# Performance work log

Measured on AMD Instinct MI355X. Metric: run time of the kernel, lower is better.

## Reference

```python
import jax, jax.numpy as jnp
import numpy as np

GAMMA = 0.99


def setup_inputs() -> dict:
    key = jax.random.key(0)
    ks = jax.random.split(key, 6)
    T, D, H = 65536, 1024, 1024
    s1 = 1.0 / np.sqrt(D)
    s2 = 1.0 / np.sqrt(H)
    return {
        "rewards": jax.random.normal(ks[0], (T,), jnp.float32),
        "obs": jax.random.normal(ks[1], (T, D), jnp.float32),
        "W1": jax.random.normal(ks[2], (D, H), jnp.float32) * s1,
        "b1": jnp.zeros((H,), jnp.float32),
        "W2": jax.random.normal(ks[3], (H, H), jnp.float32) * s2,
        "b2": jnp.zeros((H,), jnp.float32),
        "W3": jax.random.normal(ks[4], (H, 1), jnp.float32) * s2,
        "b3": jnp.zeros((1,), jnp.float32),
    }


def _discounted_returns(rewards):
    # G[i] = r[i] + gamma * G[i+1], computed as a reverse scan
    def step(g, r):
        g = r + GAMMA * g
        return g, g
    _, G = jax.lax.scan(step, jnp.zeros((), rewards.dtype), rewards, reverse=True)
    return G


def reference(rewards, obs, W1, b1, W2, b2, W3, b3):
    G = _discounted_returns(rewards)              # [T]
    h = jax.nn.relu(obs @ W1 + b1)                # [T, H]
    h = jax.nn.relu(h @ W2 + b2)                  # [T, H]
    V = (h @ W3 + b3).reshape(-1)                 # [T]
    return G - V
```

## Files before the change

### kernel.cpp

```cpp
#include <hip/hip_runtime.h>

typedef __bf16 bf16x8 __attribute__((ext_vector_type(8)));
typedef __bf16 bf16x4 __attribute__((ext_vector_type(4)));
typedef float  f32x4  __attribute__((ext_vector_type(4)));

#define GAMMA 0.99f

__device__ __forceinline__ void gload_lds16(const void* g, void* l) {
  __builtin_amdgcn_global_load_lds(
      (const __attribute__((address_space(1))) void*)g,
      (__attribute__((address_space(3))) void*)l, 16, 0, 0);
}

#define VMCNT0() asm volatile("s_waitcnt vmcnt(0)" ::: "memory")
#define BAR() __builtin_amdgcn_s_barrier()
#define MFMA(d, a, b) d = __builtin_amdgcn_mfma_f32_16x16x32_bf16(a, b, d, 0, 0, 0)

__global__ __launch_bounds__(1024) void mega_prep(
    const float* __restrict__ rw, float* __restrict__ G,
    const float* __restrict__ obs, __bf16* __restrict__ obsb,
    const float* __restrict__ W1, const float* __restrict__ W2,
    __bf16* __restrict__ BT1, __bf16* __restrict__ BT2, int nObs) {
  __shared__ float smem[4224];
  const int blk = blockIdx.x;
  const int t = threadIdx.x;
  if (blk == 0) {
    float* sv = smem;
    const float4* rp = (const float4*)(rw + t * 64);
    float4 lv[16];
#pragma unroll
    for (int i = 0; i < 16; ++i) lv[i] = rp[i];
    float loc[64];
#pragma unroll
    for (int i = 0; i < 16; ++i) {
      loc[4 * i + 0] = lv[i].x; loc[4 * i + 1] = lv[i].y;
      loc[4 * i + 2] = lv[i].z; loc[4 * i + 3] = lv[i].w;
    }
    float g = 0.f;
#pragma unroll
    for (int j = 63; j >= 0; --j) { g = loc[j] + GAMMA * g; loc[j] = g; }
    sv[t] = g;
    float W = GAMMA;
#pragma unroll
    for (int i = 0; i < 6; ++i) W *= W;
    float v = g;
    for (int s = 1; s < 1024; s <<= 1) {
      __syncthreads();
      float o = (t + s < 1024) ? sv[t + s] : 0.f;
      __syncthreads();
      v += W * o;
      sv[t] = v;
      W *= W;
    }
    __syncthreads();
    const float nxt = (t < 1023) ? sv[t + 1] : 0.f;
    float pw = GAMMA;
#pragma unroll
    for (int j = 63; j >= 0; --j) {
      G[t * 64 + j] = loc[j] + pw * nxt;
      pw *= GAMMA;
    }
  } else if (blk <= nObs) {
    const size_t base = (size_t)(blk - 1) * 32768 + (size_t)t * 8;
#pragma unroll
    for (int it = 0; it < 4; ++it) {
      const size_t e = base + (size_t)it * 8192;
      float4 u0 = *(const float4*)(obs + e);
      float4 u1 = *(const float4*)(obs + e + 4);
      bf16x8 o = {(__bf16)u0.x, (__bf16)u0.y, (__bf16)u0.z, (__bf16)u0.w,
                  (__bf16)u1.x, (__bf16)u1.y, (__bf16)u1.z, (__bf16)u1.w};
      *(bf16x8*)(obsb + e) = o;
    }
  } else {
    const int sub = t >> 8, tt = t & 255;
    const int wi = (blk - nObs - 1) * 4 + sub;
    const float* W = (wi >= 1024) ? W2 : W1;
    __bf16* O = (wi >= 1024) ? BT2 : BT1;
    const int tile = wi & 1023;
    const int ti = tile >> 5, tj = tile & 31;
    float* s = smem + sub * 1056;
    const int rr = tt >> 3, c4 = (tt & 7) * 4;
    float4 v = *(const float4*)(W + (size_t)(ti * 32 + rr) * 1024 + tj * 32 + c4);
    s[rr * 33 + c4 + 0] = v.x; s[rr * 33 + c4 + 1] = v.y;
    s[rr * 33 + c4 + 2] = v.z; s[rr * 33 + c4 + 3] = v.w;
    __syncthreads();
    bf16x4 o = {(__bf16)s[(c4 + 0) * 33 + rr], (__bf16)s[(c4 + 1) * 33 + rr],
                (__bf16)s[(c4 + 2) * 33 + rr], (__bf16)s[(c4 + 3) * 33 + rr]};
    *(bf16x4*)(O + (size_t)(tj * 32 + rr) * 1024 + ti * 32 + c4) = o;
  }
}

#define GEMM_KLOOP(APTR, BPTR)                                                 \
  extern __shared__ char lds[];                                                \
  const int t = threadIdx.x, lane = t & 63, w = t >> 6;                        \
  const int wsr = w >> 2, wsc = w & 3, g = lane >> 4, l15 = lane & 15;         \
  const int bid = blockIdx.x;                                                  \
  const int mb = (bid & 7) * 32 + ((bid >> 3) >> 2);                           \
  const int nb = (bid >> 3) & 3;                                               \
  const size_t stg_off =                                                       \
      (size_t)(t >> 2) * 2048 + (size_t)(((t & 3) ^ ((t >> 3) & 3)) * 16);     \
  const char* Ag = (const char*)(APTR) + (size_t)mb * 524288 + stg_off;        \
  const char* Bg = (const char*)(BPTR) + (size_t)nb * 524288 + stg_off;        \
  const int csw = (g ^ ((l15 >> 1) & 3)) << 4;                                 \
  const int arb = (wsr * 64 + l15) * 64 + csw;                                 \
  const int brb = (wsc * 32 + l15) * 64 + csw + 16384;                         \
  f32x4 acc[2][4][2][2];                                                       \
  const f32x4 zero = {0.f, 0.f, 0.f, 0.f};                                     \
  _Pragma("unroll") for (int a_ = 0; a_ < 2; ++a_)                             \
  _Pragma("unroll") for (int b_ = 0; b_ < 4; ++b_)                             \
  _Pragma("unroll") for (int c_ = 0; c_ < 2; ++c_)                             \
  _Pragma("unroll") for (int d_ = 0; d_ < 2; ++d_)                             \
    acc[a_][b_][c_][d_] = zero;                                                \
  auto STA = [&](int buf, int kt) {                                            \
    const char* s = Ag + kt * 64;                                              \
    char* d = lds + buf * 32768 + t * 16;                                      \
    gload_lds16(s, d);                                                         \
    gload_lds16(s + 262144, d + 8192);                                         \
  };                                                                           \
  auto STB = [&](int buf, int kt) {                                            \
    const char* s = Bg + kt * 64;                                              \
    char* d = lds + buf * 32768 + 16384 + t * 16;                              \
    gload_lds16(s, d);                                                         \
    gload_lds16(s + 262144, d + 8192);                                         \
  };                                                                           \
  STA(0, 0);                                                                   \
  STB(0, 0);                                                                   \
  VMCNT0();                                                                    \
  BAR();                                                                       \
  int cur = 0;                                                                 \
  for (int kt = 0; kt < 32; ++kt) {                                            \
    const int nx = cur ^ 1;                                                    \
    const char* ab = lds + cur * 32768;                                        \
    if (kt < 31) STA(nx, kt + 1);                                              \
    bf16x8 bfr[2][2];                                                          \
    _Pragma("unroll") for (int nh = 0; nh < 2; ++nh)                           \
    _Pragma("unroll") for (int j = 0; j < 2; ++j)                              \
      bfr[nh][j] = *(const bf16x8*)(ab + brb + (nh * 128 + j * 16) * 64);      \
    if (kt < 31) STB(nx, kt + 1);                                              \
    bf16x8 afr[4];                                                             \
    _Pragma("unroll") for (int i = 0; i < 4; ++i)                              \
      afr[i] = *(const bf16x8*)(ab + arb + (i * 16) * 64);                     \
    __builtin_amdgcn_s_setprio(1);                                             \
    _Pragma("unroll") for (int i = 0; i < 4; ++i)                              \
    _Pragma("unroll") for (int nh = 0; nh < 2; ++nh)                           \
    _Pragma("unroll") for (int j = 0; j < 2; ++j)                              \
      MFMA(acc[0][i][nh][j], bfr[nh][j], afr[i]);                              \
    __builtin_amdgcn_s_setprio(0);                                             \
    _Pragma("unroll") for (int i = 0; i < 4; ++i)                              \
      afr[i] = *(const bf16x8*)(ab + arb + ((128 + i * 16) * 64));             \
    __builtin_amdgcn_s_setprio(1);                                             \
    _Pragma("unroll") for (int i = 0; i < 4; ++i)                              \
    _Pragma("unroll") for (int nh = 0; nh < 2; ++nh)                           \
    _Pragma("unroll") for (int j = 0; j < 2; ++j)                              \
      MFMA(acc[1][i][nh][j], bfr[nh][j], afr[i]);                              \
    __builtin_amdgcn_s_setprio(0);                                             \
    if (kt < 31) VMCNT0();                                                     \
    BAR();                                                                     \
    cur = nx;                                                                  \
  }

__global__ __launch_bounds__(512, 2) void gemm1(
    const __bf16* __restrict__ obsb, const __bf16* __restrict__ BT1,
    const float* __restrict__ b1, __bf16* __restrict__ h1) {
  GEMM_KLOOP(obsb, BT1)
  f32x4 b1q[2][2];
#pragma unroll
  for (int nh = 0; nh < 2; ++nh)
#pragma unroll
    for (int j = 0; j < 2; ++j)
      b1q[nh][j] =
          *(const f32x4*)(b1 + nb * 256 + nh * 128 + wsc * 32 + j * 16 + g * 4);
#pragma unroll
  for (int mh = 0; mh < 2; ++mh)
#pragma unroll
    for (int i = 0; i < 4; ++i) {
      const size_t mrow = (size_t)(mb * 256 + mh * 128 + wsr * 64 + i * 16 + l15);
#pragma unroll
      for (int nh = 0; nh < 2; ++nh)
#pragma unroll
        for (int j = 0; j < 2; ++j) {
          f32x4 v = acc[mh][i][nh][j];
          v.x += b1q[nh][j].x; v.y += b1q[nh][j].y;
          v.z += b1q[nh][j].z; v.w += b1q[nh][j].w;
          v.x = v.x > 0.f ? v.x : 0.f;
          v.y = v.y > 0.f ? v.y : 0.f;
          v.z = v.z > 0.f ? v.z : 0.f;
          v.w = v.w > 0.f ? v.w : 0.f;
          bf16x4 o = {(__bf16)v.x, (__bf16)v.y, (__bf16)v.z, (__bf16)v.w};
          *(bf16x4*)(h1 + mrow * 1024 + nb * 256 + nh * 128 + wsc * 32 +
                     j * 16 + g * 4) = o;
        }
    }
}

__global__ __launch_bounds__(512, 2) void gemm2(
    const __bf16* __restrict__ h1, const __bf16* __restrict__ BT2,
    const float* __restrict__ b2, const float* __restrict__ W3,
    float* __restrict__ V4) {
  GEMM_KLOOP(h1, BT2)
  f32x4 b2q[2][2], w3q[2][2];
#pragma unroll
  for (int nh = 0; nh < 2; ++nh)
#pragma unroll
    for (int j = 0; j < 2; ++j) {
      const int C = nb * 256 + nh * 128 + wsc * 32 + j * 16 + g * 4;
      b2q[nh][j] = *(const f32x4*)(b2 + C);
      w3q[nh][j] = *(const f32x4*)(W3 + C);
    }
  float p[2][4];
#pragma unroll
  for (int mh = 0; mh < 2; ++mh)
#pragma unroll
    for (int i = 0; i < 4; ++i) {
      float s = 0.f;
#pragma unroll
      for (int nh = 0; nh < 2; ++nh)
#pragma unroll
        for (int j = 0; j < 2; ++j) {
          f32x4 v = acc[mh][i][nh][j];
          v.x += b2q[nh][j].x; v.y += b2q[nh][j].y;
          v.z += b2q[nh][j].z; v.w += b2q[nh][j].w;
          v.x = v.x > 0.f ? v.x : 0.f;
          v.y = v.y > 0.f ? v.y : 0.f;
          v.z = v.z > 0.f ? v.z : 0.f;
          v.w = v.w > 0.f ? v.w : 0.f;
          s += v.x * w3q[nh][j].x + v.y * w3q[nh][j].y +
               v.z * w3q[nh][j].z + v.w * w3q[nh][j].w;
        }
      p[mh][i] = s;
    }
#pragma unroll
  for (int mh = 0; mh < 2; ++mh)
#pragma unroll
    for (int i = 0; i < 4; ++i) {
      p[mh][i] += __shfl_xor(p[mh][i], 16, 64);
      p[mh][i] += __shfl_xor(p[mh][i], 32, 64);
    }
  float* vp = (float*)lds;
  if (g == 0) {
#pragma unroll
    for (int mh = 0; mh < 2; ++mh)
#pragma unroll
      for (int i = 0; i < 4; ++i)
        vp[wsc * 256 + mh * 128 + wsr * 64 + i * 16 + l15] = p[mh][i];
  }
  __syncthreads();
  if (t < 256) {
    float s = vp[t] + vp[256 + t] + vp[512 + t] + vp[768 + t];
    V4[(size_t)nb * 65536 + mb * 256 + t] = s;
  }
}

__global__ __launch_bounds__(256) void final_kernel(const float* __restrict__ G,
                                                    const float* __restrict__ V4,
                                                    const float* __restrict__ b3,
                                                    float* __restrict__ out) {
  int i = blockIdx.x * 256 + threadIdx.x;
  out[i] = G[i] - (V4[i] + V4[65536 + i] + V4[131072 + i] + V4[196608 + i] + b3[0]);
}

extern "C" void kernel_launch(void* const* d_in, const int* in_sizes, int n_in,
                              void* d_out, int out_size, void* d_ws, size_t ws_size,
                              hipStream_t stream) {
  const float* rewards = (const float*)d_in[0];
  const float* obs = (const float*)d_in[1];
  const float* W1 = (const float*)d_in[2];
  const float* b1 = (const float*)d_in[3];
  const float* W2 = (const float*)d_in[4];
  const float* b2 = (const float*)d_in[5];
  const float* W3 = (const float*)d_in[6];
  const float* b3 = (const float*)d_in[7];
  float* out = (float*)d_out;

  char* ws = (char*)d_ws;
  __bf16* BT1 = (__bf16*)(ws);
  __bf16* BT2 = (__bf16*)(ws + (2u << 20));
  float* V4 = (float*)(ws + (4u << 20));
  float* G = (float*)(ws + (5u << 20));
  __bf16* obsb = (__bf16*)(ws + (8u << 20));
  __bf16* h1 = (__bf16*)(ws + (136u << 20));

  hipFuncSetAttribute((const void*)gemm1,
                      hipFuncAttributeMaxDynamicSharedMemorySize, 65536);
  hipFuncSetAttribute((const void*)gemm2,
                      hipFuncAttributeMaxDynamicSharedMemorySize, 65536);

  mega_prep<<<1 + 2048 + 512, 1024, 0, stream>>>(rewards, G, obs, obsb, W1, W2,
                                                 BT1, BT2, 2048);
  gemm1<<<1024, 512, 65536, stream>>>(obsb, BT1, b1, h1);
  gemm2<<<1024, 512, 65536, stream>>>(h1, BT2, b2, W3, V4);
  final_kernel<<<256, 256, 0, stream>>>(G, V4, b3, out);
}
```

Baseline: 357.7 us.

## Fuse obs bf16 conversion into gemm1 and triple-buffer GEMM k-loops

Removes the separate fp32→bf16 pass over obs. gemm1 now loads fp32 obs rows into registers, converts them and writes them to LDS itself. Both GEMMs move from double to triple LDS buffering with two stages in flight and partial vmcnt waits, and the discounted-return scan moves into an extra gemm1 block. This avoids writing and re-reading a 128MB bf16 copy of obs and should hide more load latency. In exchange LDS per block rises to 96KB, which may cut occupancy, and the A-operand path in gemm1 now uses register loads instead of direct global-to-LDS loads.

```diff
diff --git a/kernel.cpp b/kernel.cpp
--- a/kernel.cpp
+++ b/kernel.cpp
@@ -12,85 +12,36 @@
       (__attribute__((address_space(3))) void*)l, 16, 0, 0);
 }
 
-#define VMCNT0() asm volatile("s_waitcnt vmcnt(0)" ::: "memory")
+#define VMCNT(n) asm volatile("s_waitcnt vmcnt(" #n ")" ::: "memory")
+#define LGKM0()                                         \
+  do {                                                  \
+    asm volatile("s_waitcnt lgkmcnt(0)" ::: "memory");  \
+    __builtin_amdgcn_sched_barrier(0);                  \
+  } while (0)
 #define BAR() __builtin_amdgcn_s_barrier()
 #define MFMA(d, a, b) d = __builtin_amdgcn_mfma_f32_16x16x32_bf16(a, b, d, 0, 0, 0)
 
-__global__ __launch_bounds__(1024) void mega_prep(
-    const float* __restrict__ rw, float* __restrict__ G,
-    const float* __restrict__ obs, __bf16* __restrict__ obsb,
-    const float* __restrict__ W1, const float* __restrict__ W2,
-    __bf16* __restrict__ BT1, __bf16* __restrict__ BT2, int nObs) {
-  __shared__ float smem[4224];
-  const int blk = blockIdx.x;
+__global__ __launch_bounds__(256) void prep_w(const float* __restrict__ W1,
+                                              const float* __restrict__ W2,
+                                              __bf16* __restrict__ BT1,
+                                              __bf16* __restrict__ BT2) {
+  const int bx = blockIdx.x;
+  const float* W = (bx >= 1024) ? W2 : W1;
+  __bf16* O = (bx >= 1024) ? BT2 : BT1;
+  const int tile = bx & 1023;
+  const int ti = tile >> 5, tj = tile & 31;
+  __shared__ float s[32][33];
   const int t = threadIdx.x;
-  if (blk == 0) {
-    float* sv = smem;
-    const float4* rp = (const float4*)(rw + t * 64);
-    float4 lv[16];
-#pragma unroll
-    for (int i = 0; i < 16; ++i) lv[i] = rp[i];
-    float loc[64];
-#pragma unroll
-    for (int i = 0; i < 16; ++i) {
-      loc[4 * i + 0] = lv[i].x; loc[4 * i + 1] = lv[i].y;
-      loc[4 * i + 2] = lv[i].z; loc[4 * i + 3] = lv[i].w;
-    }
-    float g = 0.f;
-#pragma unroll
-    for (int j = 63; j >= 0; --j) { g = loc[j] + GAMMA * g; loc[j] = g; }
-    sv[t] = g;
-    float W = GAMMA;
-#pragma unroll
-    for (int i = 0; i < 6; ++i) W *= W;
-    float v = g;
-    for (int s = 1; s < 1024; s <<= 1) {
-      __syncthreads();
-      float o = (t + s < 1024) ? sv[t + s] : 0.f;
-      __syncthreads();
-      v += W * o;
-      sv[t] = v;
-      W *= W;
-    }
-    __syncthreads();
-    const float nxt = (t < 1023) ? sv[t + 1] : 0.f;
-    float pw = GAMMA;
-#pragma unroll
-    for (int j = 63; j >= 0; --j) {
-      G[t * 64 + j] = loc[j] + pw * nxt;
-      pw *= GAMMA;
-    }
-  } else if (blk <= nObs) {
-    const size_t base = (size_t)(blk - 1) * 32768 + (size_t)t * 8;
-#pragma unroll
-    for (int it = 0; it < 4; ++it) {
-      const size_t e = base + (size_t)it * 8192;
-      float4 u0 = *(const float4*)(obs + e);
-      float4 u1 = *(const float4*)(obs + e + 4);
-      bf16x8 o = {(__bf16)u0.x, (__bf16)u0.y, (__bf16)u0.z, (__bf16)u0.w,
-                  (__bf16)u1.x, (__bf16)u1.y, (__bf16)u1.z, (__bf16)u1.w};
-      *(bf16x8*)(obsb + e) = o;
-    }
-  } else {
-    const int sub = t >> 8, tt = t & 255;
-    const int wi = (blk - nObs - 1) * 4 + sub;
-    const float* W = (wi >= 1024) ? W2 : W1;
-    __bf16* O = (wi >= 1024) ? BT2 : BT1;
-    const int tile = wi & 1023;
-    const int ti = tile >> 5, tj = tile & 31;
-    float* s = smem + sub * 1056;
-    const int rr = tt >> 3, c4 = (tt & 7) * 4;
-    float4 v = *(const float4*)(W + (size_t)(ti * 32 + rr) * 1024 + tj * 32 + c4);
-    s[rr * 33 + c4 + 0] = v.x; s[rr * 33 + c4 + 1] = v.y;
-    s[rr * 33 + c4 + 2] = v.z; s[rr * 33 + c4 + 3] = v.w;
-    __syncthreads();
-    bf16x4 o = {(__bf16)s[(c4 + 0) * 33 + rr], (__bf16)s[(c4 + 1) * 33 + rr],
-                (__bf16)s[(c4 + 2) * 33 + rr], (__bf16)s[(c4 + 3) * 33 + rr]};
-    *(bf16x4*)(O + (size_t)(tj * 32 + rr) * 1024 + ti * 32 + c4) = o;
-  }
-}
-
-#define GEMM_KLOOP(APTR, BPTR)                                                 \
+  const int rr = t >> 3, c4 = (t & 7) * 4;
+  float4 v = *(const float4*)(W + (size_t)(ti * 32 + rr) * 1024 + tj * 32 + c4);
+  s[rr][c4 + 0] = v.x; s[rr][c4 + 1] = v.y; s[rr][c4 + 2] = v.z; s[rr][c4 + 3] = v.w;
+  __syncthreads();
+  bf16x4 o = {(__bf16)s[c4 + 0][rr], (__bf16)s[c4 + 1][rr],
+              (__bf16)s[c4 + 2][rr], (__bf16)s[c4 + 3][rr]};
+  *(bf16x4*)(O + (size_t)(tj * 32 + rr) * 1024 + ti * 32 + c4) = o;
+}
+
+#define GEMM_SETUP(APTR, BPTR)                                                 \
   extern __shared__ char lds[];                                                \
   const int t = threadIdx.x, lane = t & 63, w = t >> 6;                        \
   const int wsr = w >> 2, wsc = w & 3, g = lane >> 4, l15 = lane & 15;         \
@@ -99,7 +50,6 @@
   const int nb = (bid >> 3) & 3;                                               \
   const size_t stg_off =                                                       \
       (size_t)(t >> 2) * 2048 + (size_t)(((t & 3) ^ ((t >> 3) & 3)) * 16);     \
-  const char* Ag = (const char*)(APTR) + (size_t)mb * 524288 + stg_off;        \
   const char* Bg = (const char*)(BPTR) + (size_t)nb * 524288 + stg_off;        \
   const int csw = (g ^ ((l15 >> 1) & 3)) << 4;                                 \
   const int arb = (wsr * 64 + l15) * 64 + csw;                                 \
@@ -111,33 +61,21 @@
   _Pragma("unroll") for (int c_ = 0; c_ < 2; ++c_)                             \
   _Pragma("unroll") for (int d_ = 0; d_ < 2; ++d_)                             \
     acc[a_][b_][c_][d_] = zero;                                                \
-  auto STA = [&](int buf, int kt) {                                            \
-    const char* s = Ag + kt * 64;                                              \
-    char* d = lds + buf * 32768 + t * 16;                                      \
-    gload_lds16(s, d);                                                         \
-    gload_lds16(s + 262144, d + 8192);                                         \
-  };                                                                           \
   auto STB = [&](int buf, int kt) {                                            \
     const char* s = Bg + kt * 64;                                              \
     char* d = lds + buf * 32768 + 16384 + t * 16;                              \
     gload_lds16(s, d);                                                         \
     gload_lds16(s + 262144, d + 8192);                                         \
   };                                                                           \
-  STA(0, 0);                                                                   \
-  STB(0, 0);                                                                   \
-  VMCNT0();                                                                    \
-  BAR();                                                                       \
-  int cur = 0;                                                                 \
-  for (int kt = 0; kt < 32; ++kt) {                                            \
-    const int nx = cur ^ 1;                                                    \
-    const char* ab = lds + cur * 32768;                                        \
-    if (kt < 31) STA(nx, kt + 1);                                              \
-    bf16x8 bfr[2][2];                                                          \
+  (void)0
+
+#define COMPUTE(BC)                                                            \
+  do {                                                                         \
+    const char* ab = lds + (BC) * 32768;                                       \
+    bf16x8 bfr[2][2], afr[4];                                                  \
     _Pragma("unroll") for (int nh = 0; nh < 2; ++nh)                           \
     _Pragma("unroll") for (int j = 0; j < 2; ++j)                              \
       bfr[nh][j] = *(const bf16x8*)(ab + brb + (nh * 128 + j * 16) * 64);      \
-    if (kt < 31) STB(nx, kt + 1);                                              \
-    bf16x8 afr[4];                                                             \
     _Pragma("unroll") for (int i = 0; i < 4; ++i)                              \
       afr[i] = *(const bf16x8*)(ab + arb + (i * 16) * 64);                     \
     __builtin_amdgcn_s_setprio(1);                                             \
@@ -154,15 +92,112 @@
     _Pragma("unroll") for (int j = 0; j < 2; ++j)                              \
       MFMA(acc[1][i][nh][j], bfr[nh][j], afr[i]);                              \
     __builtin_amdgcn_s_setprio(0);                                             \
-    if (kt < 31) VMCNT0();                                                     \
+  } while (0)
+
+__global__ __launch_bounds__(512, 2) void gemm1(
+    const float* __restrict__ obs, const __bf16* __restrict__ BT1,
+    const float* __restrict__ b1, __bf16* __restrict__ h1,
+    const float* __restrict__ rw, float* __restrict__ G) {
+  extern __shared__ char lds0[];
+  if (blockIdx.x == 1024) {
+    float* sv = (float*)lds0;
+    const int t = threadIdx.x;
+    const float4* rp = (const float4*)(rw + t * 128);
+    float loc[128];
+#pragma unroll
+    for (int i = 0; i < 32; ++i) {
+      float4 v = rp[i];
+      loc[4 * i + 0] = v.x; loc[4 * i + 1] = v.y;
+      loc[4 * i + 2] = v.z; loc[4 * i + 3] = v.w;
+    }
+    float gg = 0.f;
+#pragma unroll
+    for (int j = 127; j >= 0; --j) { gg = loc[j] + GAMMA * gg; loc[j] = gg; }
+    sv[t] = gg;
+    float W = GAMMA;
+#pragma unroll
+    for (int i = 0; i < 7; ++i) W *= W;
+    float v = gg;
+    for (int s = 1; s < 512; s <<= 1) {
+      __syncthreads();
+      float o = (t + s < 512) ? sv[t + s] : 0.f;
+      __syncthreads();
+      v += W * o;
+      sv[t] = v;
+      W *= W;
+    }
+    __syncthreads();
+    const float nxt = (t < 511) ? sv[t + 1] : 0.f;
+    float pw = GAMMA;
+#pragma unroll
+    for (int j = 127; j >= 0; --j) {
+      G[t * 128 + j] = loc[j] + pw * nxt;
+      pw *= GAMMA;
+    }
+    return;
+  }
+  GEMM_SETUP(obs, BT1);
+  const int ra = t >> 1, ha = t & 1;
+  const float4* Ap =
+      (const float4*)(obs + (size_t)(mb * 256 + ra) * 1024 + ha * 16);
+  const int aq = (ra >> 1) & 3;
+  const int slot0 = (2 * ha) ^ aq;
+  char* awbase = lds + ra * 64;
+  auto WRA = [&](int buf, const float4* R) {
+    bf16x8 w0 = {(__bf16)R[0].x, (__bf16)R[0].y, (__bf16)R[0].z, (__bf16)R[0].w,
+                 (__bf16)R[1].x, (__bf16)R[1].y, (__bf16)R[1].z, (__bf16)R[1].w};
+    bf16x8 w1 = {(__bf16)R[2].x, (__bf16)R[2].y, (__bf16)R[2].z, (__bf16)R[2].w,
+                 (__bf16)R[3].x, (__bf16)R[3].y, (__bf16)R[3].z, (__bf16)R[3].w};
+    *(bf16x8*)(awbase + buf * 32768 + slot0 * 16) = w0;
+    *(bf16x8*)(awbase + buf * 32768 + (slot0 ^ 1) * 16) = w1;
+  };
+  float4 avP[4], avQ[4];
+#pragma unroll
+  for (int i = 0; i < 4; ++i) avP[i] = Ap[i];
+  STB(0, 0);
+#pragma unroll
+  for (int i = 0; i < 4; ++i) avQ[i] = Ap[8 + i];
+  STB(1, 1);
+  VMCNT(8);
+  WRA(0, avP);
+  int bc = 0;
+
+#define G1_ITER(KT, RL, RW, VM)                                                \
+  do {                                                                         \
+    int bs = bc + 2; if (bs >= 3) bs -= 3;                                     \
+    int bw = bc + 1; if (bw >= 3) bw -= 3;                                     \
+    _Pragma("unroll") for (int i_ = 0; i_ < 4; ++i_)                           \
+      RL[i_] = Ap[(KT + 2) * 8 + i_];                                          \
+    STB(bs, (KT + 2));                                                         \
+    VMCNT(VM);                                                                 \
+    WRA(bw, RW);                                                               \
+    LGKM0();                                                                   \
     BAR();                                                                     \
-    cur = nx;                                                                  \
-  }
-
-__global__ __launch_bounds__(512, 2) void gemm1(
-    const __bf16* __restrict__ obsb, const __bf16* __restrict__ BT1,
-    const float* __restrict__ b1, __bf16* __restrict__ h1) {
-  GEMM_KLOOP(obsb, BT1)
+    COMPUTE(bc);                                                               \
+    BAR();                                                                     \
+    bc = bw;                                                                   \
+  } while (0)
+
+  for (int u = 0; u < 15; ++u) {
+    const int k0 = 2 * u;
+    G1_ITER(k0, avP, avQ, 8);
+    G1_ITER((k0 + 1), avQ, avP, 8);
+  }
+  {
+    int bw = bc + 1; if (bw >= 3) bw -= 3;
+    VMCNT(2);
+    WRA(bw, avQ);
+    LGKM0();
+    BAR();
+    COMPUTE(bc);
+    BAR();
+    bc = bw;
+  }
+  VMCNT(0);
+  BAR();
+  COMPUTE(bc);
+#undef G1_ITER
+
   f32x4 b1q[2][2];
 #pragma unroll
   for (int nh = 0; nh < 2; ++nh)
@@ -197,7 +232,40 @@
     const __bf16* __restrict__ h1, const __bf16* __restrict__ BT2,
     const float* __restrict__ b2, const float* __restrict__ W3,
     float* __restrict__ V4) {
-  GEMM_KLOOP(h1, BT2)
+  GEMM_SETUP(h1, BT2);
+  const char* Ag = (const char*)h1 + (size_t)mb * 524288 + stg_off;
+  auto STA = [&](int buf, int kt) {
+    const char* s = Ag + kt * 64;
+    char* d = lds + buf * 32768 + t * 16;
+    gload_lds16(s, d);
+    gload_lds16(s + 262144, d + 8192);
+  };
+  STA(0, 0); STB(0, 0);
+  STA(1, 1); STB(1, 1);
+  int bc = 0;
+  for (int kt = 0; kt < 30; ++kt) {
+    int bs = bc + 2; if (bs >= 3) bs -= 3;
+    int bw = bc + 1; if (bw >= 3) bw -= 3;
+    STA(bs, kt + 2);
+    STB(bs, kt + 2);
+    VMCNT(8);
+    BAR();
+    COMPUTE(bc);
+    BAR();
+    bc = bw;
+  }
+  {
+    int bw = bc + 1; if (bw >= 3) bw -= 3;
+    VMCNT(4);
+    BAR();
+    COMPUTE(bc);
+    BAR();
+    bc = bw;
+  }
+  VMCNT(0);
+  BAR();
+  COMPUTE(bc);
+
   f32x4 b2q[2][2], w3q[2][2];
 #pragma unroll
   for (int nh = 0; nh < 2; ++nh)
@@ -277,17 +345,15 @@
   __bf16* BT2 = (__bf16*)(ws + (2u << 20));
   float* V4 = (float*)(ws + (4u << 20));
   float* G = (float*)(ws + (5u << 20));
-  __bf16* obsb = (__bf16*)(ws + (8u << 20));
-  __bf16* h1 = (__bf16*)(ws + (136u << 20));
+  __bf16* h1 = (__bf16*)(ws + (8u << 20));
 
   hipFuncSetAttribute((const void*)gemm1,
-                      hipFuncAttributeMaxDynamicSharedMemorySize, 65536);
+                      hipFuncAttributeMaxDynamicSharedMemorySize, 98304);
   hipFuncSetAttribute((const void*)gemm2,
-                      hipFuncAttributeMaxDynamicSharedMemorySize, 65536);
-
-  mega_prep<<<1 + 2048 + 512, 1024, 0, stream>>>(rewards, G, obs, obsb, W1, W2,
-                                                 BT1, BT2, 2048);
-  gemm1<<<1024, 512, 65536, stream>>>(obsb, BT1, b1, h1);
-  gemm2<<<1024, 512, 65536, stream>>>(h1, BT2, b2, W3, V4);
+                      hipFuncAttributeMaxDynamicSharedMemorySize, 98304);
+
+  prep_w<<<2048, 256, 0, stream>>>(W1, W2, BT1, BT2);
+  gemm1<<<1025, 512, 98304, stream>>>(obs, BT1, b1, h1, rewards, G);
+  gemm2<<<1024, 512, 98304, stream>>>(h1, BT2, b2, W3, V4);
   final_kernel<<<256, 256, 0, stream>>>(G, V4, b3, out);
 }
```

Result: slower. 436.2 us (+21.9%).

## Triple-buffer GEMM k-loop with prefetch depth two and partial vmcnt waits

Applied to the files above, without the earlier changes.

Replaces the double-buffered LDS pipeline in both GEMMs with a three-stage ring that issues loads two k-tiles ahead. It waits with vmcnt(8) so only the oldest tile must have landed, instead of draining all loads every iteration. LDS per block grows from 64KB to 96KB. With launch bounds of 2 blocks per CU, this may cut occupancy if the CU's LDS cannot hold two such blocks. It also adds a second barrier per iteration. The prep kernel's nObs parameter is hardcoded as a constant.

```diff
diff --git a/kernel.cpp b/kernel.cpp
--- a/kernel.cpp
+++ b/kernel.cpp
@@ -12,7 +12,7 @@
       (__attribute__((address_space(3))) void*)l, 16, 0, 0);
 }
 
-#define VMCNT0() asm volatile("s_waitcnt vmcnt(0)" ::: "memory")
+#define VMCNT(n) asm volatile("s_waitcnt vmcnt(" #n ")" ::: "memory")
 #define BAR() __builtin_amdgcn_s_barrier()
 #define MFMA(d, a, b) d = __builtin_amdgcn_mfma_f32_16x16x32_bf16(a, b, d, 0, 0, 0)
 
@@ -20,7 +20,7 @@
     const float* __restrict__ rw, float* __restrict__ G,
     const float* __restrict__ obs, __bf16* __restrict__ obsb,
     const float* __restrict__ W1, const float* __restrict__ W2,
-    __bf16* __restrict__ BT1, __bf16* __restrict__ BT2, int nObs) {
+    __bf16* __restrict__ BT1, __bf16* __restrict__ BT2) {
   __shared__ float smem[4224];
   const int blk = blockIdx.x;
   const int t = threadIdx.x;
@@ -60,7 +60,7 @@
       G[t * 64 + j] = loc[j] + pw * nxt;
       pw *= GAMMA;
     }
-  } else if (blk <= nObs) {
+  } else if (blk <= 2048) {
     const size_t base = (size_t)(blk - 1) * 32768 + (size_t)t * 8;
 #pragma unroll
     for (int it = 0; it < 4; ++it) {
@@ -73,7 +73,7 @@
     }
   } else {
     const int sub = t >> 8, tt = t & 255;
-    const int wi = (blk - nObs - 1) * 4 + sub;
+    const int wi = (blk - 2049) * 4 + sub;
     const float* W = (wi >= 1024) ? W2 : W1;
     __bf16* O = (wi >= 1024) ? BT2 : BT1;
     const int tile = wi & 1023;
@@ -123,21 +123,12 @@
     gload_lds16(s, d);                                                         \
     gload_lds16(s + 262144, d + 8192);                                         \
   };                                                                           \
-  STA(0, 0);                                                                   \
-  STB(0, 0);                                                                   \
-  VMCNT0();                                                                    \
-  BAR();                                                                       \
-  int cur = 0;                                                                 \
-  for (int kt = 0; kt < 32; ++kt) {                                            \
-    const int nx = cur ^ 1;                                                    \
-    const char* ab = lds + cur * 32768;                                        \
-    if (kt < 31) STA(nx, kt + 1);                                              \
-    bf16x8 bfr[2][2];                                                          \
+  auto COMPUTE = [&](int bc) {                                                 \
+    const char* ab = lds + bc * 32768;                                         \
+    bf16x8 bfr[2][2], afr[4];                                                  \
     _Pragma("unroll") for (int nh = 0; nh < 2; ++nh)                           \
     _Pragma("unroll") for (int j = 0; j < 2; ++j)                              \
       bfr[nh][j] = *(const bf16x8*)(ab + brb + (nh * 128 + j * 16) * 64);      \
-    if (kt < 31) STB(nx, kt + 1);                                              \
-    bf16x8 afr[4];                                                             \
     _Pragma("unroll") for (int i = 0; i < 4; ++i)                              \
       afr[i] = *(const bf16x8*)(ab + arb + (i * 16) * 64);                     \
     __builtin_amdgcn_s_setprio(1);                                             \
@@ -154,10 +145,32 @@
     _Pragma("unroll") for (int j = 0; j < 2; ++j)                              \
       MFMA(acc[1][i][nh][j], bfr[nh][j], afr[i]);                              \
     __builtin_amdgcn_s_setprio(0);                                             \
-    if (kt < 31) VMCNT0();                                                     \
+  };                                                                           \
+  STA(0, 0); STB(0, 0);                                                        \
+  STA(1, 1); STB(1, 1);                                                        \
+  int bc = 0;                                                                  \
+  for (int kt = 0; kt < 30; ++kt) {                                            \
+    int bs = bc + 2; if (bs >= 3) bs -= 3;                                     \
+    int bw = bc + 1; if (bw >= 3) bw -= 3;                                     \
+    STA(bs, kt + 2);                                                           \
+    STB(bs, kt + 2);                                                           \
+    VMCNT(8);                                                                  \
     BAR();                                                                     \
-    cur = nx;                                                                  \
-  }
+    COMPUTE(bc);                                                               \
+    BAR();                                                                     \
+    bc = bw;                                                                   \
+  }                                                                            \
+  {                                                                            \
+    int bw = bc + 1; if (bw >= 3) bw -= 3;                                     \
+    VMCNT(4);                                                                  \
+    BAR();                                                                     \
+    COMPUTE(bc);                                                               \
+    BAR();                                                                     \
+    bc = bw;                                                                   \
+  }                                                                            \
+  VMCNT(0);                                                                    \
+  BAR();                                                                       \
+  COMPUTE(bc);
 
 __global__ __launch_bounds__(512, 2) void gemm1(
     const __bf16* __restrict__ obsb, const __bf16* __restrict__ BT1,
@@ -281,13 +294,12 @@
   __bf16* h1 = (__bf16*)(ws + (136u << 20));
 
   hipFuncSetAttribute((const void*)gemm1,
-                      hipFuncAttributeMaxDynamicSharedMemorySize, 65536);
+                      hipFuncAttributeMaxDynamicSharedMemorySize, 98304);
   hipFuncSetAttribute((const void*)gemm2,
-                      hipFuncAttributeMaxDynamicSharedMemorySize, 65536);
-
-  mega_prep<<<1 + 2048 + 512, 1024, 0, stream>>>(rewards, G, obs, obsb, W1, W2,
-                                                 BT1, BT2, 2048);
-  gemm1<<<1024, 512, 65536, stream>>>(obsb, BT1, b1, h1);
-  gemm2<<<1024, 512, 65536, stream>>>(h1, BT2, b2, W3, V4);
+                      hipFuncAttributeMaxDynamicSharedMemorySize, 98304);
+
+  mega_prep<<<2561, 1024, 0, stream>>>(rewards, G, obs, obsb, W1, W2, BT1, BT2);
+  gemm1<<<1024, 512, 98304, stream>>>(obsb, BT1, b1, h1);
+  gemm2<<<1024, 512, 98304, stream>>>(h1, BT2, b2, W3, V4);
   final_kernel<<<256, 256, 0, stream>>>(G, V4, b3, out);
 }
```

Measured after the change: 354.0 us. No clear change (-1.0%).

## Fuse fp32-to-bf16 obs conversion into gemm1 and deepen LDS pipelining

Applied to the files above, without the earlier changes.

Removes the separate obs fp32→bf16 conversion pass and has gemm1 stage fp32 obs tiles straight into LDS, converting to bf16 when loading MFMA fragments. This avoids writing and re-reading a 128MB bf16 copy of obs. gemm1 moves to a 3-stage buffer ring and gemm2 to a 4-stage ring, with partial vmcnt waits so more loads are in flight. In exchange, LDS use per block rises to 144KB and 128KB, which can limit occupancy below the requested 2 blocks per CU. gemm1 also reads twice the A bytes from global memory and does the conversion in its inner loop.

```diff
diff --git a/kernel.cpp b/kernel.cpp
--- a/kernel.cpp
+++ b/kernel.cpp
@@ -12,15 +12,14 @@
       (__attribute__((address_space(3))) void*)l, 16, 0, 0);
 }
 
-#define VMCNT0() asm volatile("s_waitcnt vmcnt(0)" ::: "memory")
+#define VMCNT(n) asm volatile("s_waitcnt vmcnt(" #n ")" ::: "memory")
 #define BAR() __builtin_amdgcn_s_barrier()
 #define MFMA(d, a, b) d = __builtin_amdgcn_mfma_f32_16x16x32_bf16(a, b, d, 0, 0, 0)
 
-__global__ __launch_bounds__(1024) void mega_prep(
+__global__ __launch_bounds__(1024) void prep(
     const float* __restrict__ rw, float* __restrict__ G,
-    const float* __restrict__ obs, __bf16* __restrict__ obsb,
     const float* __restrict__ W1, const float* __restrict__ W2,
-    __bf16* __restrict__ BT1, __bf16* __restrict__ BT2, int nObs) {
+    __bf16* __restrict__ BT1, __bf16* __restrict__ BT2) {
   __shared__ float smem[4224];
   const int blk = blockIdx.x;
   const int t = threadIdx.x;
@@ -60,20 +59,9 @@
       G[t * 64 + j] = loc[j] + pw * nxt;
       pw *= GAMMA;
     }
-  } else if (blk <= nObs) {
-    const size_t base = (size_t)(blk - 1) * 32768 + (size_t)t * 8;
-#pragma unroll
-    for (int it = 0; it < 4; ++it) {
-      const size_t e = base + (size_t)it * 8192;
-      float4 u0 = *(const float4*)(obs + e);
-      float4 u1 = *(const float4*)(obs + e + 4);
-      bf16x8 o = {(__bf16)u0.x, (__bf16)u0.y, (__bf16)u0.z, (__bf16)u0.w,
-                  (__bf16)u1.x, (__bf16)u1.y, (__bf16)u1.z, (__bf16)u1.w};
-      *(bf16x8*)(obsb + e) = o;
-    }
   } else {
     const int sub = t >> 8, tt = t & 255;
-    const int wi = (blk - nObs - 1) * 4 + sub;
+    const int wi = (blk - 1) * 4 + sub;
     const float* W = (wi >= 1024) ? W2 : W1;
     __bf16* O = (wi >= 1024) ? BT2 : BT1;
     const int tile = wi & 1023;
@@ -90,79 +78,116 @@
   }
 }
 
-#define GEMM_KLOOP(APTR, BPTR)                                                 \
-  extern __shared__ char lds[];                                                \
-  const int t = threadIdx.x, lane = t & 63, w = t >> 6;                        \
-  const int wsr = w >> 2, wsc = w & 3, g = lane >> 4, l15 = lane & 15;         \
-  const int bid = blockIdx.x;                                                  \
-  const int mb = (bid & 7) * 32 + ((bid >> 3) >> 2);                           \
-  const int nb = (bid >> 3) & 3;                                               \
-  const size_t stg_off =                                                       \
-      (size_t)(t >> 2) * 2048 + (size_t)(((t & 3) ^ ((t >> 3) & 3)) * 16);     \
-  const char* Ag = (const char*)(APTR) + (size_t)mb * 524288 + stg_off;        \
-  const char* Bg = (const char*)(BPTR) + (size_t)nb * 524288 + stg_off;        \
-  const int csw = (g ^ ((l15 >> 1) & 3)) << 4;                                 \
-  const int arb = (wsr * 64 + l15) * 64 + csw;                                 \
-  const int brb = (wsc * 32 + l15) * 64 + csw + 16384;                         \
-  f32x4 acc[2][4][2][2];                                                       \
-  const f32x4 zero = {0.f, 0.f, 0.f, 0.f};                                     \
-  _Pragma("unroll") for (int a_ = 0; a_ < 2; ++a_)                             \
-  _Pragma("unroll") for (int b_ = 0; b_ < 4; ++b_)                             \
-  _Pragma("unroll") for (int c_ = 0; c_ < 2; ++c_)                             \
-  _Pragma("unroll") for (int d_ = 0; d_ < 2; ++d_)                             \
-    acc[a_][b_][c_][d_] = zero;                                                \
-  auto STA = [&](int buf, int kt) {                                            \
-    const char* s = Ag + kt * 64;                                              \
-    char* d = lds + buf * 32768 + t * 16;                                      \
-    gload_lds16(s, d);                                                         \
-    gload_lds16(s + 262144, d + 8192);                                         \
-  };                                                                           \
-  auto STB = [&](int buf, int kt) {                                            \
-    const char* s = Bg + kt * 64;                                              \
-    char* d = lds + buf * 32768 + 16384 + t * 16;                              \
-    gload_lds16(s, d);                                                         \
-    gload_lds16(s + 262144, d + 8192);                                         \
-  };                                                                           \
-  STA(0, 0);                                                                   \
-  STB(0, 0);                                                                   \
-  VMCNT0();                                                                    \
-  BAR();                                                                       \
-  int cur = 0;                                                                 \
-  for (int kt = 0; kt < 32; ++kt) {                                            \
-    const int nx = cur ^ 1;                                                    \
-    const char* ab = lds + cur * 32768;                                        \
-    if (kt < 31) STA(nx, kt + 1);                                              \
-    bf16x8 bfr[2][2];                                                          \
-    _Pragma("unroll") for (int nh = 0; nh < 2; ++nh)                           \
-    _Pragma("unroll") for (int j = 0; j < 2; ++j)                              \
-      bfr[nh][j] = *(const bf16x8*)(ab + brb + (nh * 128 + j * 16) * 64);      \
-    if (kt < 31) STB(nx, kt + 1);                                              \
-    bf16x8 afr[4];                                                             \
-    _Pragma("unroll") for (int i = 0; i < 4; ++i)                              \
-      afr[i] = *(const bf16x8*)(ab + arb + (i * 16) * 64);                     \
-    __builtin_amdgcn_s_setprio(1);                                             \
-    _Pragma("unroll") for (int i = 0; i < 4; ++i)                              \
-    _Pragma("unroll") for (int nh = 0; nh < 2; ++nh)                           \
-    _Pragma("unroll") for (int j = 0; j < 2; ++j)                              \
-      MFMA(acc[0][i][nh][j], bfr[nh][j], afr[i]);                              \
-    __builtin_amdgcn_s_setprio(0);                                             \
-    _Pragma("unroll") for (int i = 0; i < 4; ++i)                              \
-      afr[i] = *(const bf16x8*)(ab + arb + ((128 + i * 16) * 64));             \
-    __builtin_amdgcn_s_setprio(1);                                             \
-    _Pragma("unroll") for (int i = 0; i < 4; ++i)                              \
-    _Pragma("unroll") for (int nh = 0; nh < 2; ++nh)                           \
-    _Pragma("unroll") for (int j = 0; j < 2; ++j)                              \
-      MFMA(acc[1][i][nh][j], bfr[nh][j], afr[i]);                              \
-    __builtin_amdgcn_s_setprio(0);                                             \
-    if (kt < 31) VMCNT0();                                                     \
-    BAR();                                                                     \
-    cur = nx;                                                                  \
+__global__ __launch_bounds__(512, 2) void gemm1(
+    const float* __restrict__ obs, const __bf16* __restrict__ BT1,
+    const float* __restrict__ b1, __bf16* __restrict__ h1) {
+  extern __shared__ char lds[];
+  const int t = threadIdx.x, lane = t & 63, w = t >> 6;
+  const int wsr = w >> 2, wsc = w & 3, g = lane >> 4, l15 = lane & 15;
+  const int bid = blockIdx.x;
+  const int mb = (bid & 7) * 32 + ((bid >> 3) >> 2);
+  const int nb = (bid >> 3) & 3;
+
+  const size_t stg_off =
+      (size_t)(t >> 2) * 2048 + (size_t)(((t & 3) ^ ((t >> 3) & 3)) * 16);
+  const char* Bg = (const char*)BT1 + (size_t)nb * 524288 + stg_off;
+  const char* Asrc = (const char*)obs +
+      ((size_t)(mb * 256 + w * 32 + (lane >> 3)) * 4096) +
+      (size_t)(16 * ((lane & 7) ^ (lane >> 3)));
+  const int aldst = w * 4096 + lane * 16;
+
+  const int csw = (g ^ ((l15 >> 1) & 3)) << 4;
+  const int brb = (wsc * 32 + l15) * 64 + csw;
+
+  f32x4 acc[2][4][2][2];
+  const f32x4 zero = {0.f, 0.f, 0.f, 0.f};
+#pragma unroll
+  for (int a_ = 0; a_ < 2; ++a_)
+#pragma unroll
+    for (int b_ = 0; b_ < 4; ++b_)
+#pragma unroll
+      for (int c_ = 0; c_ < 2; ++c_)
+#pragma unroll
+        for (int d_ = 0; d_ < 2; ++d_) acc[a_][b_][c_][d_] = zero;
+
+  auto STA = [&](int buf, int kt) {
+    const char* s = Asrc + kt * 128;
+    char* d = lds + buf * 49152 + aldst;
+    gload_lds16(s, d);
+    gload_lds16(s + 32768, d + 1024);
+    gload_lds16(s + 65536, d + 2048);
+    gload_lds16(s + 98304, d + 3072);
+  };
+  auto STB = [&](int buf, int kt) {
+    const char* s = Bg + kt * 64;
+    char* d = lds + buf * 49152 + 32768 + t * 16;
+    gload_lds16(s, d);
+    gload_lds16(s + 262144, d + 8192);
+  };
+  auto LDAF = [&](const char* ab, int r) -> bf16x8 {
+    const int o1 = (g * 32) ^ ((r & 7) << 4);
+    const f32x4 a0 = *(const f32x4*)(ab + r * 128 + o1);
+    const f32x4 a1 = *(const f32x4*)(ab + r * 128 + (o1 ^ 16));
+    bf16x8 v = {(__bf16)a0[0], (__bf16)a0[1], (__bf16)a0[2], (__bf16)a0[3],
+                (__bf16)a1[0], (__bf16)a1[1], (__bf16)a1[2], (__bf16)a1[3]};
+    return v;
+  };
+  auto COMPUTE = [&](int bc) {
+    const char* ab = lds + bc * 49152;
+    const char* bb = ab + 32768;
+    bf16x8 bfr[2][2], afr[4];
+#pragma unroll
+    for (int nh = 0; nh < 2; ++nh)
+#pragma unroll
+      for (int j = 0; j < 2; ++j)
+        bfr[nh][j] = *(const bf16x8*)(bb + brb + (nh * 128 + j * 16) * 64);
+#pragma unroll
+    for (int i = 0; i < 4; ++i) afr[i] = LDAF(ab, wsr * 64 + 16 * i + l15);
+    __builtin_amdgcn_s_setprio(1);
+#pragma unroll
+    for (int i = 0; i < 4; ++i)
+#pragma unroll
+      for (int nh = 0; nh < 2; ++nh)
+#pragma unroll
+        for (int j = 0; j < 2; ++j)
+          MFMA(acc[0][i][nh][j], bfr[nh][j], afr[i]);
+    __builtin_amdgcn_s_setprio(0);
+#pragma unroll
+    for (int i = 0; i < 4; ++i)
+      afr[i] = LDAF(ab, 128 + wsr * 64 + 16 * i + l15);
+    __builtin_amdgcn_s_setprio(1);
+#pragma unroll
+    for (int i = 0; i < 4; ++i)
+#pragma unroll
+      for (int nh = 0; nh < 2; ++nh)
+#pragma unroll
+        for (int j = 0; j < 2; ++j)
+          MFMA(acc[1][i][nh][j], bfr[nh][j], afr[i]);
+    __builtin_amdgcn_s_setprio(0);
+  };
+
+  STA(0, 0); STB(0, 0);
+  STA(1, 1); STB(1, 1);
+  int bc = 0;
+  for (int kt = 0; kt < 30; ++kt) {
+    int bs = bc + 2; if (bs >= 3) bs -= 3;
+    STA(bs, kt + 2);
+    STB(bs, kt + 2);
+    VMCNT(12);
+    BAR();
+    COMPUTE(bc);
+    BAR();
+    bc = bc + 1; if (bc >= 3) bc -= 3;
   }
-
-__global__ __launch_bounds__(512, 2) void gemm1(
-    const __bf16* __restrict__ obsb, const __bf16* __restrict__ BT1,
-    const float* __restrict__ b1, __bf16* __restrict__ h1) {
-  GEMM_KLOOP(obsb, BT1)
+  VMCNT(6);
+  BAR();
+  COMPUTE(bc);
+  BAR();
+  bc = bc + 1; if (bc >= 3) bc -= 3;
+  VMCNT(0);
+  BAR();
+  COMPUTE(bc);
+
   f32x4 b1q[2][2];
 #pragma unroll
   for (int nh = 0; nh < 2; ++nh)
@@ -197,7 +222,105 @@
     const __bf16* __restrict__ h1, const __bf16* __restrict__ BT2,
     const float* __restrict__ b2, const float* __restrict__ W3,
     float* __restrict__ V4) {
-  GEMM_KLOOP(h1, BT2)
+  extern __shared__ char lds[];
+  const int t = threadIdx.x, lane = t & 63, w = t >> 6;
+  const int wsr = w >> 2, wsc = w & 3, g = lane >> 4, l15 = lane & 15;
+  const int bid = blockIdx.x;
+  const int mb = (bid & 7) * 32 + ((bid >> 3) >> 2);
+  const int nb = (bid >> 3) & 3;
+  const size_t stg_off =
+      (size_t)(t >> 2) * 2048 + (size_t)(((t & 3) ^ ((t >> 3) & 3)) * 16);
+  const char* Ag = (const char*)h1 + (size_t)mb * 524288 + stg_off;
+  const char* Bg = (const char*)BT2 + (size_t)nb * 524288 + stg_off;
+  const int csw = (g ^ ((l15 >> 1) & 3)) << 4;
+  const int arb = (wsr * 64 + l15) * 64 + csw;
+  const int brb = (wsc * 32 + l15) * 64 + csw + 16384;
+
+  f32x4 acc[2][4][2][2];
+  const f32x4 zero = {0.f, 0.f, 0.f, 0.f};
+#pragma unroll
+  for (int a_ = 0; a_ < 2; ++a_)
+#pragma unroll
+    for (int b_ = 0; b_ < 4; ++b_)
+#pragma unroll
+      for (int c_ = 0; c_ < 2; ++c_)
+#pragma unroll
+        for (int d_ = 0; d_ < 2; ++d_) acc[a_][b_][c_][d_] = zero;
+
+  auto STA = [&](int buf, int kt) {
+    const char* s = Ag + kt * 64;
+    char* d = lds + buf * 32768 + t * 16;
+    gload_lds16(s, d);
+    gload_lds16(s + 262144, d + 8192);
+  };
+  auto STB = [&](int buf, int kt) {
+    const char* s = Bg + kt * 64;
+    char* d = lds + buf * 32768 + 16384 + t * 16;
+    gload_lds16(s, d);
+    gload_lds16(s + 262144, d + 8192);
+  };
+  auto COMPUTE = [&](int bc) {
+    const char* ab = lds + bc * 32768;
+    bf16x8 bfr[2][2], afr[4];
+#pragma unroll
+    for (int nh = 0; nh < 2; ++nh)
+#pragma unroll
+      for (int j = 0; j < 2; ++j)
+        bfr[nh][j] = *(const bf16x8*)(ab + brb + (nh * 128 + j * 16) * 64);
+#pragma unroll
+    for (int i = 0; i < 4; ++i)
+      afr[i] = *(const bf16x8*)(ab + arb + (i * 16) * 64);
+    __builtin_amdgcn_s_setprio(1);
+#pragma unroll
+    for (int i = 0; i < 4; ++i)
+#pragma unroll
+      for (int nh = 0; nh < 2; ++nh)
+#pragma unroll
+        for (int j = 0; j < 2; ++j)
+          MFMA(acc[0][i][nh][j], bfr[nh][j], afr[i]);
+    __builtin_amdgcn_s_setprio(0);
+#pragma unroll
+    for (int i = 0; i < 4; ++i)
+      afr[i] = *(const bf16x8*)(ab + arb + ((128 + i * 16) * 64));
+    __builtin_amdgcn_s_setprio(1);
+#pragma unroll
+    for (int i = 0; i < 4; ++i)
+#pragma unroll
+      for (int nh = 0; nh < 2; ++nh)
+#pragma unroll
+        for (int j = 0; j < 2; ++j)
+          MFMA(acc[1][i][nh][j], bfr[nh][j], afr[i]);
+    __builtin_amdgcn_s_setprio(0);
+  };
+
+  STA(0, 0); STB(0, 0);
+  STA(1, 1); STB(1, 1);
+  STA(2, 2); STB(2, 2);
+  int bc = 0;
+  for (int kt = 0; kt < 29; ++kt) {
+    int bs = bc + 3; if (bs >= 4) bs -= 4;
+    STA(bs, kt + 3);
+    STB(bs, kt + 3);
+    VMCNT(12);
+    BAR();
+    COMPUTE(bc);
+    BAR();
+    bc = (bc + 1) & 3;
+  }
+  VMCNT(8);
+  BAR();
+  COMPUTE(bc);
+  BAR();
+  bc = (bc + 1) & 3;
+  VMCNT(4);
+  BAR();
+  COMPUTE(bc);
+  BAR();
+  bc = (bc + 1) & 3;
+  VMCNT(0);
+  BAR();
+  COMPUTE(bc);
+
   f32x4 b2q[2][2], w3q[2][2];
 #pragma unroll
   for (int nh = 0; nh < 2; ++nh)
@@ -277,17 +400,15 @@
   __bf16* BT2 = (__bf16*)(ws + (2u << 20));
   float* V4 = (float*)(ws + (4u << 20));
   float* G = (float*)(ws + (5u << 20));
-  __bf16* obsb = (__bf16*)(ws + (8u << 20));
-  __bf16* h1 = (__bf16*)(ws + (136u << 20));
+  __bf16* h1 = (__bf16*)(ws + (8u << 20));
 
   hipFuncSetAttribute((const void*)gemm1,
-                      hipFuncAttributeMaxDynamicSharedMemorySize, 65536);
+                      hipFuncAttributeMaxDynamicSharedMemorySize, 147456);
   hipFuncSetAttribute((const void*)gemm2,
-                      hipFuncAttributeMaxDynamicSharedMemorySize, 65536);
-
-  mega_prep<<<1 + 2048 + 512, 1024, 0, stream>>>(rewards, G, obs, obsb, W1, W2,
-                                                 BT1, BT2, 2048);
-  gemm1<<<1024, 512, 65536, stream>>>(obsb, BT1, b1, h1);
-  gemm2<<<1024, 512, 65536, stream>>>(h1, BT2, b2, W3, V4);
+                      hipFuncAttributeMaxDynamicSharedMemorySize, 131072);
+
+  prep<<<513, 1024, 0, stream>>>(rewards, G, W1, W2, BT1, BT2);
+  gemm1<<<1024, 512, 147456, stream>>>(obs, BT1, b1, h1);
+  gemm2<<<1024, 512, 131072, stream>>>(h1, BT2, b2, W3, V4);
   final_kernel<<<256, 256, 0, stream>>>(G, V4, b3, out);
 }
```

After: 370.5 us. 1.04x slower.
